# Kernel optimization log

Measured on AMD Instinct MI355X. Metric: run time of the kernel, lower is better.

## Reference

```python
import jax, jax.numpy as jnp
import numpy as np

DIM = 512
CODEBOOK_SIZE = 2048
NUM_Q = 8
COMMIT_W = 0.25
B, T = 8, 2048


def setup_inputs() -> dict:
    key = jax.random.key(0)
    k1, k2 = jax.random.split(key)
    x = jax.random.normal(k1, (B, T, DIM), dtype=jnp.float32)
    lim = 1.0 / CODEBOOK_SIZE
    codebooks = jax.random.uniform(k2, (NUM_Q, CODEBOOK_SIZE, DIM), dtype=jnp.float32,
                                   minval=-lim, maxval=lim)
    return {"x": x, "codebooks": codebooks}


def reference(x, codebooks):
    """Residual VQ forward.
    x: (B, T, D); codebooks: (Q, K, D).
    Returns (quantized (B,T,D), indices (B,T,Q) int32, mean loss scalar).
    """
    sg = jax.lax.stop_gradient
    residual = x
    quantized = jnp.zeros_like(x)
    idx_list = []
    total_loss = jnp.zeros((), dtype=x.dtype)
    for i in range(NUM_Q):
        cb = codebooks[i]  # (K, D)
        # squared L2 distances: (B,T,K)
        d = (jnp.sum(residual * residual, axis=-1, keepdims=True)
             - 2.0 * jnp.einsum('btd,kd->btk', residual, cb)
             + jnp.sum(cb * cb, axis=-1))
        min_idx = jnp.argmin(d, axis=-1)  # (B,T)
        idx_list.append(min_idx)
        q_lvl = cb[min_idx]  # (B,T,D) gather
        quantized = quantized + q_lvl
        commit_loss = jnp.mean((sg(residual) - q_lvl) ** 2)
        codebook_loss = jnp.mean((residual - sg(q_lvl)) ** 2)
        total_loss = total_loss + commit_loss * COMMIT_W + codebook_loss
        residual = residual - sg(q_lvl)
    # straight-through estimator
    quantized = x + sg(quantized - x)
    indices = jnp.stack(idx_list, axis=-1)  # (B,T,Q)
    return quantized, indices, total_loss / NUM_Q
```

## Files before the change

kernel.cpp:

```cpp
#include <hip/hip_runtime.h>


constexpr int DIM   = 512;
constexpr int KCB   = 2048;
constexpr int NQ    = 8;
constexpr int NTOK  = 8 * 2048;
constexpr int QELEM = NTOK * DIM;
constexpr int NBLK2 = KCB / 256;
constexpr float WINDOW = 1e-3f;

using short8  = __attribute__((ext_vector_type(8))) short;
using float4v = __attribute__((ext_vector_type(4))) float;

__device__ __forceinline__ unsigned short f2bf(float f) {
    unsigned u = __float_as_uint(f);
    return (unsigned short)((u + 0x7FFFu + ((u >> 16) & 1u)) >> 16);
}

__device__ __forceinline__ void gl2lds16(const void* g, void* l) {
    __builtin_amdgcn_global_load_lds(
        (__attribute__((address_space(1))) void*)g,
        (__attribute__((address_space(3))) void*)l, 16, 0, 0);
}

struct Top4 { float s[4]; int i[4]; };
__device__ __forceinline__ void t4_init(Top4& t) {
#pragma unroll
    for (int j = 0; j < 4; ++j) { t.s[j] = 3.0e38f; t.i[j] = 0x7FFFFFFF; }
}
__device__ __forceinline__ void t4_ins(Top4& t, float s, int idx) {
    if (s < t.s[3]) {
        if (s < t.s[2]) { t.s[3] = t.s[2]; t.i[3] = t.i[2];
            if (s < t.s[1]) { t.s[2] = t.s[1]; t.i[2] = t.i[1];
                if (s < t.s[0]) { t.s[1] = t.s[0]; t.i[1] = t.i[0]; t.s[0] = s; t.i[0] = idx; }
                else            { t.s[1] = s; t.i[1] = idx; }
            } else { t.s[2] = s; t.i[2] = idx; }
        } else { t.s[3] = s; t.i[3] = idx; }
    }
}

__global__ __launch_bounds__(256) void k_initnorm(
        const float* __restrict__ x, const float* __restrict__ cbs,
        float4* __restrict__ R, ushort4* __restrict__ Rb, ushort4* __restrict__ Cbb,
        float* __restrict__ r2, float* __restrict__ c2)
{
#pragma clang fp contract(off)
    __shared__ float buf[4][DIM];
    __shared__ float accs[4][32];
    const int w = threadIdx.x >> 6, lane = threadIdx.x & 63;
    const bool isX = blockIdx.x < (NTOK / 4);
    const int row = (isX ? blockIdx.x : blockIdx.x - NTOK / 4) * 4 + w;

    const float* src = isX ? x : cbs;
    const float4* a4 = reinterpret_cast<const float4*>(src + (size_t)row * DIM);
    float4 v0 = a4[lane], v1 = a4[lane + 64];

    ushort4 b0 = make_ushort4(f2bf(v0.x), f2bf(v0.y), f2bf(v0.z), f2bf(v0.w));
    ushort4 b1 = make_ushort4(f2bf(v1.x), f2bf(v1.y), f2bf(v1.z), f2bf(v1.w));
    if (isX) {
        R [(size_t)row * 128 + lane]      = v0;
        R [(size_t)row * 128 + lane + 64] = v1;
        Rb[(size_t)row * 128 + lane]      = b0;
        Rb[(size_t)row * 128 + lane + 64] = b1;
    } else {
        Cbb[(size_t)row * 128 + lane]      = b0;
        Cbb[(size_t)row * 128 + lane + 64] = b1;
    }

    float4* b4 = reinterpret_cast<float4*>(buf[w]);
    b4[lane]      = v0;
    b4[lane + 64] = v1;
    __syncthreads();
    if (lane < 32) {
        int blk = lane >> 3, j = lane & 7;
        const float* p = buf[w] + blk * 128 + j;
        float x0 = p[0];
        float acc = x0 * x0;
#pragma unroll
        for (int m = 1; m < 16; ++m) { float xx = p[8 * m]; acc = acc + xx * xx; }
        accs[w][lane] = acc;
    }
    __syncthreads();
    if (lane == 0) {
        float B[4];
#pragma unroll
        for (int blk = 0; blk < 4; ++blk) {
            const float* r = &accs[w][blk * 8];
            B[blk] = ((r[0] + r[1]) + (r[2] + r[3])) + ((r[4] + r[5]) + (r[6] + r[7]));
        }
        float out = (B[0] + B[1]) + (B[2] + B[3]);
        if (isX) r2[row] = out; else c2[row] = out;
    }
}

__global__ __launch_bounds__(512, 2) void k_gemm_topk(
        const unsigned short* __restrict__ Rb, const unsigned short* __restrict__ Cbb,
        const float* __restrict__ c2, float* __restrict__ candS, int* __restrict__ candI)
{
    __shared__ __align__(16) char smem[67712];
    unsigned short* As = (unsigned short*)smem;
    unsigned short* Bs = (unsigned short*)(smem + 32768);
    float*  scb = (float*)smem;
    float*  c2s = (float*)(smem + 66560);

    const int tid  = threadIdx.x;
    const int wid  = tid >> 6, lane = tid & 63;
    const int quad = lane >> 4, l16 = lane & 15;
    const int wr = wid >> 2, wc = wid & 3;

    const int L    = blockIdx.y * NBLK2 + blockIdx.x;
    const int slot = L >> 3;
    const int mb   = (L & 7) * 8 + (slot >> 3);
    const int nb2  = slot & 7;

    const int tok0 = mb * 256, n0 = nb2 * 256;

    if (tid < 256) c2s[tid + 4 * (tid >> 5)] = c2[n0 + tid];

    float4v acc[8][4];
    float4v zero = {0.f, 0.f, 0.f, 0.f};
#pragma unroll
    for (int mi = 0; mi < 8; ++mi)
#pragma unroll
        for (int nj = 0; nj < 4; ++nj) acc[mi][nj] = zero;

    auto stage = [&](int b, int kb) {
        unsigned short* Ad = As + b * 8192;
        unsigned short* Bd = Bs + b * 8192;
#pragma unroll
        for (int c = 0; c < 2; ++c) {
            int g = wid * 2 + c;
            gl2lds16(&Rb[(size_t)(tok0 + g * 16 + l16) * DIM + kb + quad * 8],
                     Ad + (size_t)g * 512);
        }
#pragma unroll
        for (int c = 0; c < 2; ++c) {
            int g = wid * 2 + c;
            gl2lds16(&Cbb[(size_t)(n0 + g * 16 + l16) * DIM + kb + quad * 8],
                     Bd + (size_t)g * 512);
        }
    };

    auto compute = [&](int b) {
        const unsigned short* Ac = As + b * 8192;
        const unsigned short* Bc = Bs + b * 8192;
        short8 af[8], bf[4];
#pragma unroll
        for (int mi = 0; mi < 8; ++mi)
            af[mi] = *(const short8*)(Ac + (size_t)(wr * 8 + mi) * 512 + lane * 8);
#pragma unroll
        for (int nj = 0; nj < 4; ++nj)
            bf[nj] = *(const short8*)(Bc + (size_t)(wc * 4 + nj) * 512 + lane * 8);
        __builtin_amdgcn_s_setprio(1);
#pragma unroll
        for (int mi = 0; mi < 8; ++mi)
#pragma unroll
            for (int nj = 0; nj < 4; ++nj)
                acc[mi][nj] = __builtin_amdgcn_mfma_f32_16x16x32_bf16(
                    af[mi], bf[nj], acc[mi][nj], 0, 0, 0);
        __builtin_amdgcn_s_setprio(0);
    };

    stage(0, 0);
    for (int it = 0; it < 16; ++it) {
        __syncthreads();
        if (it < 15) stage((it + 1) & 1, (it + 1) * 32);
        compute(it & 1);
    }

    const int row_ = tid >> 3, pp = tid & 7;
    float4 c2r[8];
#pragma unroll
    for (int j = 0; j < 8; ++j)
        c2r[j] = *(const float4*)(c2s + pp * 36 + 4 * j);

#pragma unroll
    for (int qr = 0; qr < 4; ++qr) {
        __syncthreads();
        if (wr == (qr >> 1)) {
            const int mi0 = (qr & 1) * 4;
#pragma unroll
            for (int mm = 0; mm < 4; ++mm)
#pragma unroll
                for (int nj = 0; nj < 4; ++nj) {
                    int r0 = mm * 16 + quad * 4;
                    int cc = wc * 64 + nj * 16 + l16;
#pragma unroll
                    for (int e = 0; e < 4; ++e)
                        scb[(r0 + e) * 260 + cc] = acc[mi0 + mm][nj][e];
                }
        }
        __syncthreads();
        Top4 t; t4_init(t);
#pragma unroll
        for (int j = 0; j < 8; ++j) {
            float4 sv = *(const float4*)(scb + row_ * 260 + pp * 32 + 4 * j);
            float4 cv = c2r[j];
            int c0 = n0 + pp * 32 + 4 * j;
            t4_ins(t, cv.x - 2.0f * sv.x, c0 + 0);
            t4_ins(t, cv.y - 2.0f * sv.y, c0 + 1);
            t4_ins(t, cv.z - 2.0f * sv.z, c0 + 2);
            t4_ins(t, cv.w - 2.0f * sv.w, c0 + 3);
        }
#pragma unroll
        for (int k = 1; k <= 2; k <<= 1) {
            float os[4]; int oi[4];
#pragma unroll
            for (int j = 0; j < 4; ++j) {
                os[j] = __shfl_xor(t.s[j], k, 64);
                oi[j] = __shfl_xor(t.i[j], k, 64);
            }
#pragma unroll
            for (int j = 0; j < 4; ++j) t4_ins(t, os[j], oi[j]);
        }
        if ((pp & 3) == 0) {
            int token = tok0 + qr * 64 + row_;
            int nb = nb2 * 2 + (pp >> 2);
            size_t base = (size_t)token * 64 + (size_t)nb * 4;
#pragma unroll
            for (int j = 0; j < 4; ++j) { candS[base + j] = t.s[j]; candI[base + j] = t.i[j]; }
        }
    }
}

__global__ __launch_bounds__(256) void k_selupd(
        const float* __restrict__ candS, const int* __restrict__ candI,
        float* __restrict__ R, const float* __restrict__ cbf,
        float* __restrict__ r2, const float* __restrict__ c2,
        float* __restrict__ idx_out, float* __restrict__ partial,
        ushort4* __restrict__ Rb, const float4* __restrict__ x, int level)
{
#pragma clang fp contract(off)
    __shared__ float buf[4][DIM];
    __shared__ float accs[4][32];
    __shared__ float shl[4];
    const int w = threadIdx.x >> 6, lane = threadIdx.x & 63;
    const int t = blockIdx.x * 4 + w;
    const bool last = (level == NQ - 1);

    float4* r4 = reinterpret_cast<float4*>(R + (size_t)t * DIM);
    float4* b4 = reinterpret_cast<float4*>(buf[w]);
    float4 rr[2];
    rr[0] = r4[lane];      rr[1] = r4[lane + 64];
    b4[lane] = rr[0];      b4[lane + 64] = rr[1];

    float sb = candS[(size_t)t * 64 + lane];
    int   ci = candI[(size_t)t * 64 + lane];
    float mn = sb;
#pragma unroll
    for (int off = 32; off; off >>= 1) mn = fminf(mn, __shfl_xor(mn, off, 64));
    unsigned long long mask = __ballot(sb <= mn + WINDOW);
    int ncand = __popcll(mask);
    int winner;
    if (ncand == 1) {
        winner = __shfl(ci, __ffsll(mask) - 1, 64);
    } else {
        int src = 0;
        if (lane < ncand) {
            unsigned long long mm = mask;
            for (int z = 0; z < lane; ++z) mm &= mm - 1;
            src = __ffsll(mm) - 1;
        }
        int cidx = __shfl(ci, src, 64);
        float s = 3.0e38f;
        int   si = 0x7FFFFFFF;
        if (lane < ncand) {
            const float4* cp4 = reinterpret_cast<const float4*>(cbf + (size_t)cidx * DIM);
            const float4* rp4 = reinterpret_cast<const float4*>(buf[w]);
            float d = 0.f;
#pragma unroll 4
            for (int j = 0; j < DIM / 4; ++j) {
                float4 cv = cp4[j];
                float4 rv = rp4[j];
                d = fmaf(rv.x, cv.x, d);
                d = fmaf(rv.y, cv.y, d);
                d = fmaf(rv.z, cv.z, d);
                d = fmaf(rv.w, cv.w, d);
            }
            float td = 2.0f * d;
            float a  = r2[t] - td;
            s  = a + c2[cidx];
            si = cidx;
        }
#pragma unroll
        for (int off = 32; off; off >>= 1) {
            float ov = __shfl_xor(s, off, 64);
            int   oi = __shfl_xor(si, off, 64);
            if (ov < s || (ov == s && oi < si)) { s = ov; si = oi; }
        }
        winner = si;
    }
    if (lane == 0) idx_out[(size_t)t * NQ + level] = (float)winner;

    const float4* c4 = reinterpret_cast<const float4*>(cbf + (size_t)winner * DIM);
    float ls = 0.f;
#pragma unroll
    for (int i = 0; i < 2; ++i) {
        int d = lane + 64 * i;
        float4 rv = rr[i], cv = c4[d];
        rv.x -= cv.x; rv.y -= cv.y; rv.z -= cv.z; rv.w -= cv.w;
        ls = ls + rv.x * rv.x; ls = ls + rv.y * rv.y;
        ls = ls + rv.z * rv.z; ls = ls + rv.w * rv.w;
        if (!last) {
            r4[d] = rv;
            b4[d] = rv;
            Rb[(size_t)t * 128 + d] = make_ushort4(f2bf(rv.x), f2bf(rv.y),
                                                   f2bf(rv.z), f2bf(rv.w));
        } else {
            float4 xv = x[(size_t)t * 128 + d];
            xv.x -= rv.x; xv.y -= rv.y; xv.z -= rv.z; xv.w -= rv.w;
            r4[d] = xv;
        }
    }

    if (!last) {
        __syncthreads();
        if (lane < 32) {
            int blk = lane >> 3, j = lane & 7;
            const float* p = buf[w] + blk * 128 + j;
            float x0 = p[0];
            float acc = x0 * x0;
#pragma unroll
            for (int m = 1; m < 16; ++m) { float xx = p[8 * m]; acc = acc + xx * xx; }
            accs[w][lane] = acc;
        }
        __syncthreads();
        if (lane == 0) {
            float B[4];
#pragma unroll
            for (int blk = 0; blk < 4; ++blk) {
                const float* r = &accs[w][blk * 8];
                B[blk] = ((r[0] + r[1]) + (r[2] + r[3])) + ((r[4] + r[5]) + (r[6] + r[7]));
            }
            r2[t] = (B[0] + B[1]) + (B[2] + B[3]);
        }
    }

#pragma unroll
    for (int off = 32; off; off >>= 1) ls += __shfl_down(ls, off, 64);
    if (lane == 0) shl[w] = ls;
    __syncthreads();
    if (threadIdx.x == 0) partial[blockIdx.x] = (shl[0] + shl[1]) + (shl[2] + shl[3]);
}

__global__ __launch_bounds__(256) void k_finalize_loss(const float* __restrict__ partial,
                                                       float* __restrict__ loss_out)
{
    double s = 0.0;
    for (int i = threadIdx.x; i < NQ * (NTOK / 4); i += 256) s += (double)partial[i];
#pragma unroll
    for (int off = 32; off; off >>= 1) s += __shfl_down(s, off, 64);
    __shared__ double sh[4];
    if ((threadIdx.x & 63) == 0) sh[threadIdx.x >> 6] = s;
    __syncthreads();
    if (threadIdx.x == 0) {
        double tot = (sh[0] + sh[1]) + (sh[2] + sh[3]);
        loss_out[0] = (float)(tot * 1.25 / ((double)NQ * (double)QELEM));
    }
}

extern "C" void kernel_launch(void* const* d_in, const int* in_sizes, int n_in,
                              void* d_out, int out_size, void* d_ws, size_t ws_size,
                              hipStream_t stream)
{
    const float* x   = (const float*)d_in[0];
    const float* cbs = (const float*)d_in[1];

    float* qout     = (float*)d_out;
    float* idx_out  = qout + QELEM;
    float* loss_out = idx_out + (size_t)NTOK * NQ;
    float* R        = qout;

    char* ws = (char*)d_ws;
    size_t off = 0;
    unsigned short* Rb   = (unsigned short*)(ws + off); off += (size_t)QELEM * 2;
    unsigned short* Cbb  = (unsigned short*)(ws + off); off += (size_t)QELEM * 2;
    float*          c2   = (float*)(ws + off);          off += (size_t)NQ * KCB * 4;
    float*          r2   = (float*)(ws + off);          off += (size_t)NTOK * 4;
    float*          part = (float*)(ws + off);          off += (size_t)NQ * (NTOK / 4) * 4;
    float*          candS= (float*)(ws + off);          off += (size_t)NTOK * 64 * 4;
    int*            candI= (int*)(ws + off);            off += (size_t)NTOK * 64 * 4;

    k_initnorm<<<NTOK / 4 + NQ * KCB / 4, 256, 0, stream>>>(
        x, cbs, (float4*)R, (ushort4*)Rb, (ushort4*)Cbb, r2, c2);

    for (int q = 0; q < NQ; ++q) {
        const float*          cbq  = cbs + (size_t)q * KCB * DIM;
        const unsigned short* cbbq = Cbb + (size_t)q * KCB * DIM;
        const float*          c2q  = c2 + (size_t)q * KCB;
        dim3 g(NBLK2, NTOK / 256);
        k_gemm_topk<<<g, 512, 0, stream>>>(Rb, cbbq, c2q, candS, candI);
        k_selupd<<<NTOK / 4, 256, 0, stream>>>(candS, candI, R, cbq, r2, c2q,
                                               idx_out, part + (size_t)q * (NTOK / 4),
                                               (ushort4*)Rb, (const float4*)x, q);
    }

    k_finalize_loss<<<1, 256, 0, stream>>>(part, loss_out);
}
```

Baseline: 1.027 ms.

## Shrink GEMM N-tile to 128 and triple-buffer LDS with vmcnt-based waits

The GEMM+top-k kernel now uses a 256x128 output tile instead of 256x256, doubling the grid and halving per-wave accumulators (4x4 MFMA tiles). The K-loop moves from double to triple buffering, prefetching two stages ahead and waiting with explicit s_waitcnt vmcnt plus a raw barrier rather than __syncthreads. The top-k reduction covers 16 columns per lane with an extra shuffle step and writes one candidate set per 128-column block. This trades more redundant A-tile loads and more blocks for lower register pressure and better latency hiding.

```diff
diff --git a/kernel.cpp b/kernel.cpp
--- a/kernel.cpp
+++ b/kernel.cpp
@@ -6,7 +6,7 @@
 constexpr int NQ    = 8;
 constexpr int NTOK  = 8 * 2048;
 constexpr int QELEM = NTOK * DIM;
-constexpr int NBLK2 = KCB / 256;
+constexpr int NBLKC = KCB / 128;
 constexpr float WINDOW = 1e-3f;
 
 using short8  = __attribute__((ext_vector_type(8))) short;
@@ -97,63 +97,59 @@
         const unsigned short* __restrict__ Rb, const unsigned short* __restrict__ Cbb,
         const float* __restrict__ c2, float* __restrict__ candS, int* __restrict__ candI)
 {
-    __shared__ __align__(16) char smem[67712];
+    __shared__ __align__(16) char smem[74304];
     unsigned short* As = (unsigned short*)smem;
-    unsigned short* Bs = (unsigned short*)(smem + 32768);
+    unsigned short* Bs = (unsigned short*)(smem + 49152);
     float*  scb = (float*)smem;
-    float*  c2s = (float*)(smem + 66560);
+    float*  c2s = (float*)(smem + 73728);
 
     const int tid  = threadIdx.x;
     const int wid  = tid >> 6, lane = tid & 63;
     const int quad = lane >> 4, l16 = lane & 15;
-    const int wr = wid >> 2, wc = wid & 3;
-
-    const int L    = blockIdx.y * NBLK2 + blockIdx.x;
+    const int wr = wid >> 1, wc = wid & 1;
+
+    const int L    = blockIdx.y * NBLKC + blockIdx.x;
     const int slot = L >> 3;
-    const int mb   = (L & 7) * 8 + (slot >> 3);
-    const int nb2  = slot & 7;
-
-    const int tok0 = mb * 256, n0 = nb2 * 256;
-
-    if (tid < 256) c2s[tid + 4 * (tid >> 5)] = c2[n0 + tid];
-
-    float4v acc[8][4];
+    const int mb   = (L & 7) * 8 + (slot >> 4);
+    const int nb   = slot & 15;
+
+    const int tok0 = mb * 256, n0 = nb * 128;
+
+    if (tid < 128) c2s[tid + 4 * (tid >> 5)] = c2[n0 + tid];
+
+    float4v acc[4][4];
     float4v zero = {0.f, 0.f, 0.f, 0.f};
 #pragma unroll
-    for (int mi = 0; mi < 8; ++mi)
+    for (int mi = 0; mi < 4; ++mi)
 #pragma unroll
         for (int nj = 0; nj < 4; ++nj) acc[mi][nj] = zero;
 
     auto stage = [&](int b, int kb) {
         unsigned short* Ad = As + b * 8192;
-        unsigned short* Bd = Bs + b * 8192;
+        unsigned short* Bd = Bs + b * 4096;
 #pragma unroll
         for (int c = 0; c < 2; ++c) {
-            int g = wid * 2 + c;
+            int g = wid + c * 8;
             gl2lds16(&Rb[(size_t)(tok0 + g * 16 + l16) * DIM + kb + quad * 8],
                      Ad + (size_t)g * 512);
         }
-#pragma unroll
-        for (int c = 0; c < 2; ++c) {
-            int g = wid * 2 + c;
-            gl2lds16(&Cbb[(size_t)(n0 + g * 16 + l16) * DIM + kb + quad * 8],
-                     Bd + (size_t)g * 512);
-        }
+        gl2lds16(&Cbb[(size_t)(n0 + wid * 16 + l16) * DIM + kb + quad * 8],
+                 Bd + (size_t)wid * 512);
     };
 
     auto compute = [&](int b) {
         const unsigned short* Ac = As + b * 8192;
-        const unsigned short* Bc = Bs + b * 8192;
-        short8 af[8], bf[4];
-#pragma unroll
-        for (int mi = 0; mi < 8; ++mi)
-            af[mi] = *(const short8*)(Ac + (size_t)(wr * 8 + mi) * 512 + lane * 8);
+        const unsigned short* Bc = Bs + b * 4096;
+        short8 af[4], bf[4];
+#pragma unroll
+        for (int mi = 0; mi < 4; ++mi)
+            af[mi] = *(const short8*)(Ac + (size_t)(wr * 4 + mi) * 512 + lane * 8);
 #pragma unroll
         for (int nj = 0; nj < 4; ++nj)
             bf[nj] = *(const short8*)(Bc + (size_t)(wc * 4 + nj) * 512 + lane * 8);
         __builtin_amdgcn_s_setprio(1);
 #pragma unroll
-        for (int mi = 0; mi < 8; ++mi)
+        for (int mi = 0; mi < 4; ++mi)
 #pragma unroll
             for (int nj = 0; nj < 4; ++nj)
                 acc[mi][nj] = __builtin_amdgcn_mfma_f32_16x16x32_bf16(
@@ -162,48 +158,54 @@
     };
 
     stage(0, 0);
+    stage(1, 32);
+    int cur = 0, pf = 2;
     for (int it = 0; it < 16; ++it) {
-        __syncthreads();
-        if (it < 15) stage((it + 1) & 1, (it + 1) * 32);
-        compute(it & 1);
+        if (it < 15) asm volatile("s_waitcnt vmcnt(3)" ::: "memory");
+        else         asm volatile("s_waitcnt vmcnt(0)" ::: "memory");
+        __builtin_amdgcn_s_barrier();
+        __builtin_amdgcn_sched_barrier(0);
+        if (it < 14) stage(pf, (it + 2) * 32);
+        compute(cur);
+        cur = (cur == 2) ? 0 : cur + 1;
+        pf  = (pf  == 2) ? 0 : pf  + 1;
     }
 
     const int row_ = tid >> 3, pp = tid & 7;
-    float4 c2r[8];
-#pragma unroll
-    for (int j = 0; j < 8; ++j)
-        c2r[j] = *(const float4*)(c2s + pp * 36 + 4 * j);
+    float4 c2r[4];
+#pragma unroll
+    for (int j = 0; j < 4; ++j)
+        c2r[j] = *(const float4*)(c2s + pp * 16 + 4 * (pp >> 1) + 4 * j);
 
 #pragma unroll
     for (int qr = 0; qr < 4; ++qr) {
         __syncthreads();
-        if (wr == (qr >> 1)) {
-            const int mi0 = (qr & 1) * 4;
-#pragma unroll
-            for (int mm = 0; mm < 4; ++mm)
+        if (wr == qr) {
+#pragma unroll
+            for (int mi = 0; mi < 4; ++mi)
 #pragma unroll
                 for (int nj = 0; nj < 4; ++nj) {
-                    int r0 = mm * 16 + quad * 4;
+                    int r0 = mi * 16 + quad * 4;
                     int cc = wc * 64 + nj * 16 + l16;
 #pragma unroll
                     for (int e = 0; e < 4; ++e)
-                        scb[(r0 + e) * 260 + cc] = acc[mi0 + mm][nj][e];
+                        scb[(r0 + e) * 132 + cc] = acc[mi][nj][e];
                 }
         }
         __syncthreads();
         Top4 t; t4_init(t);
 #pragma unroll
-        for (int j = 0; j < 8; ++j) {
-            float4 sv = *(const float4*)(scb + row_ * 260 + pp * 32 + 4 * j);
+        for (int j = 0; j < 4; ++j) {
+            float4 sv = *(const float4*)(scb + row_ * 132 + pp * 16 + 4 * j);
             float4 cv = c2r[j];
-            int c0 = n0 + pp * 32 + 4 * j;
+            int c0 = n0 + pp * 16 + 4 * j;
             t4_ins(t, cv.x - 2.0f * sv.x, c0 + 0);
             t4_ins(t, cv.y - 2.0f * sv.y, c0 + 1);
             t4_ins(t, cv.z - 2.0f * sv.z, c0 + 2);
             t4_ins(t, cv.w - 2.0f * sv.w, c0 + 3);
         }
 #pragma unroll
-        for (int k = 1; k <= 2; k <<= 1) {
+        for (int k = 1; k <= 4; k <<= 1) {
             float os[4]; int oi[4];
 #pragma unroll
             for (int j = 0; j < 4; ++j) {
@@ -213,9 +215,8 @@
 #pragma unroll
             for (int j = 0; j < 4; ++j) t4_ins(t, os[j], oi[j]);
         }
-        if ((pp & 3) == 0) {
+        if (pp == 0) {
             int token = tok0 + qr * 64 + row_;
-            int nb = nb2 * 2 + (pp >> 2);
             size_t base = (size_t)token * 64 + (size_t)nb * 4;
 #pragma unroll
             for (int j = 0; j < 4; ++j) { candS[base + j] = t.s[j]; candI[base + j] = t.i[j]; }
@@ -388,7 +389,7 @@
         const float*          cbq  = cbs + (size_t)q * KCB * DIM;
         const unsigned short* cbbq = Cbb + (size_t)q * KCB * DIM;
         const float*          c2q  = c2 + (size_t)q * KCB;
-        dim3 g(NBLK2, NTOK / 256);
+        dim3 g(NBLKC, NTOK / 256);
         k_gemm_topk<<<g, 512, 0, stream>>>(Rb, cbbq, c2q, candS, candI);
         k_selupd<<<NTOK / 4, 256, 0, stream>>>(candS, candI, R, cbq, r2, c2q,
                                                idx_out, part + (size_t)q * (NTOK / 4),
```

Result: slower. 1.205 ms (+17.3%).
